# Performance work log

Measured on AMD Instinct MI355X. Metric: run time of the kernel, lower is better.

Reference implementation:

```python
import jax, jax.numpy as jnp
import numpy as np

B, C, H, W = 4, 256, 64, 64
CH = C // 2  # inner channels


def setup_inputs() -> dict:
    key = jax.random.key(0)
    ks = jax.random.split(key, 9)
    s_in = 1.0 / np.sqrt(C)
    s_w = 1.0 / np.sqrt(CH)
    return {
        "x": jax.random.normal(ks[0], (B, C, H, W), dtype=jnp.float32),
        "theta_w": jax.random.normal(ks[1], (CH, C), dtype=jnp.float32) * s_in,
        "theta_b": jax.random.normal(ks[2], (CH,), dtype=jnp.float32) * s_in,
        "phi_w": jax.random.normal(ks[3], (CH, C), dtype=jnp.float32) * s_in,
        "phi_b": jax.random.normal(ks[4], (CH,), dtype=jnp.float32) * s_in,
        "g_w": jax.random.normal(ks[5], (CH, C), dtype=jnp.float32) * s_in,
        "g_b": jax.random.normal(ks[6], (CH,), dtype=jnp.float32) * s_in,
        "W_w": jax.random.normal(ks[7], (C, CH), dtype=jnp.float32) * s_w,
        "W_b": jax.random.normal(ks[8], (C,), dtype=jnp.float32) * s_w,
    }


def _proj(x_flat, w, b):
    # 1x1 conv == channel matmul; x_flat: [B, C, N] -> [B, O, N]
    return jnp.einsum("oc,bcn->bon", w, x_flat) + b[None, :, None]


def reference(x, theta_w, theta_b, phi_w, phi_b, g_w, g_b, W_w, W_b):
    b, c, h, w = x.shape
    n = h * w
    xf = x.reshape(b, c, n)
    theta = _proj(xf, theta_w, theta_b)  # [B, CH, N]
    phi = _proj(xf, phi_w, phi_b)        # [B, CH, N]
    g = _proj(xf, g_w, g_b)              # [B, CH, N]
    # scores[b,i,j] = theta[:, :, i] . phi[:, :, j]; softmax over j
    attn = jax.nn.softmax(jnp.einsum("bci,bcj->bij", theta, phi), axis=-1)
    # torch: bmm(g_x, attn) -> out[b,c,i] = sum_j g[b,c,j] * attn[b,j,i]
    out = jnp.einsum("bcj,bji->bci", g, attn)  # [B, CH, N]
    out = jnp.einsum("oc,bcn->bon", W_w, out) + W_b[None, :, None]
    return out.reshape(b, c, h, w) + x
```

## Files before the change

### kernel.cpp

```cpp
#include <hip/hip_runtime.h>
#include <hip/hip_bf16.h>
#include <math.h>

#define BB    4
#define CC    256
#define CHN   128
#define NN    4096

typedef short short8 __attribute__((ext_vector_type(8)));
typedef float f32x4  __attribute__((ext_vector_type(4)));
typedef float f32x16 __attribute__((ext_vector_type(16)));
typedef unsigned short u16;
typedef u16  us4 __attribute__((ext_vector_type(4)));

#define MFMA16(a, b, c) __builtin_amdgcn_mfma_f32_16x16x32_bf16((a), (b), (c), 0, 0, 0)
#define MFMA32(a, b, c) __builtin_amdgcn_mfma_f32_32x32x16_bf16((a), (b), (c), 0, 0, 0)
#define LOG2E 1.4426950408889634f

#if __has_builtin(__builtin_amdgcn_exp2f)
#define EXP2F(x) __builtin_amdgcn_exp2f(x)
#else
#define EXP2F(x) exp2f(x)
#endif
#if __has_builtin(__builtin_amdgcn_logf)
#define LOG2F(x) __builtin_amdgcn_logf(x)
#else
#define LOG2F(x) log2f(x)
#endif

static __device__ __forceinline__ u16 f2bf(float f) {
    union { float f; unsigned u; } v; v.f = f;
    unsigned r = v.u + 0x7FFFu + ((v.u >> 16) & 1u);
    return (u16)(r >> 16);
}
static __device__ __forceinline__ unsigned pkbf(float a, float b) {
    __hip_bfloat162 h = __float22bfloat162_rn(make_float2(a, b));
    return *reinterpret_cast<unsigned*>(&h);
}
static __device__ __forceinline__ int sw128(int row, int u) {
    return row * 128 + ((u ^ (row & 7)) << 3);
}

__global__ __launch_bounds__(256) void k_cvtw(
    const float* __restrict__ tw, const float* __restrict__ pw,
    const float* __restrict__ gw, const float* __restrict__ Ww,
    u16* __restrict__ wall)
{
    int idx = (blockIdx.x * 256 + threadIdx.x) * 4;
    const float* s = (idx < 32768) ? tw
                   : (idx < 65536) ? pw
                   : (idx < 98304) ? gw : Ww;
    float sc = (idx < 32768) ? LOG2E : 1.0f;
    float4 v = *(const float4*)(s + (idx & 32767));
    us4 r = { f2bf(v.x * sc), f2bf(v.y * sc), f2bf(v.z * sc), f2bf(v.w * sc) };
    *(us4*)(wall + idx) = r;
}

__global__ __launch_bounds__(512) void k_proj(
    const float* __restrict__ x, const u16* __restrict__ wall,
    const float* __restrict__ tb, const float* __restrict__ pb,
    const float* __restrict__ gbias,
    u16* __restrict__ tht, u16* __restrict__ pht, u16* __restrict__ gg)
{
    __shared__ u16 xs[64 * 264];
    __shared__ u16 gbuf[128 * 68];
    const int tid = threadIdx.x;
    const int n0  = blockIdx.x * 64;
    const int b   = blockIdx.y;
    const int ln  = tid & 15, q = (tid >> 4) & 3, wid = tid >> 6;
    const int ow  = wid & 1, nw = wid >> 1;

    for (int p = 0; p < 8; ++p) {
        int id = p * 512 + tid;
        int c = id >> 4, n4 = (id & 15) * 4;
        float4 xv = *(const float4*)(x + ((size_t)b * CC + c) * NN + n0 + n4);
        xs[(n4 + 0) * 264 + c] = f2bf(xv.x);
        xs[(n4 + 1) * 264 + c] = f2bf(xv.y);
        xs[(n4 + 2) * 264 + c] = f2bf(xv.z);
        xs[(n4 + 3) * 264 + c] = f2bf(xv.w);
    }
    __syncthreads();

    short8 bfr[8];
    #pragma unroll
    for (int ks = 0; ks < 8; ++ks)
        bfr[ks] = *(const short8*)(&xs[(nw * 16 + ln) * 264 + ks * 32 + q * 8]);

    for (int pr = 0; pr < 3; ++pr) {
        const u16* wsrc = wall + pr * 32768;
        f32x4 acc[4];
        #pragma unroll
        for (int oo = 0; oo < 4; ++oo) acc[oo] = (f32x4){0.f, 0.f, 0.f, 0.f};
        for (int ks = 0; ks < 8; ++ks) {
            short8 a[4];
            #pragma unroll
            for (int oo = 0; oo < 4; ++oo)
                a[oo] = *(const short8*)(wsrc + (size_t)(ow*64 + oo*16 + ln) * 256 + ks*32 + q*8);
            #pragma unroll
            for (int oo = 0; oo < 4; ++oo)
                acc[oo] = MFMA16(a[oo], bfr[ks], acc[oo]);
        }
        const float* bias = (pr == 0) ? tb : (pr == 1 ? pb : gbias);
        const float bsc = (pr == 0) ? LOG2E : 1.0f;
        if (pr < 2) {
            u16* dst = (pr == 0) ? tht : pht;
            const int n = n0 + nw * 16 + ln;
            #pragma unroll
            for (int oo = 0; oo < 4; ++oo) {
                int o = ow * 64 + oo * 16 + q * 4;
                float4 bv = *(const float4*)(bias + o);
                f32x4 v = acc[oo];
                uint2 r = { pkbf(v.x + bv.x * bsc, v.y + bv.y * bsc),
                            pkbf(v.z + bv.z * bsc, v.w + bv.w * bsc) };
                *(uint2*)(dst + ((size_t)b * NN + n) * CHN + o) = r;
            }
        } else {
            const int nl = nw * 16 + ln;
            #pragma unroll
            for (int oo = 0; oo < 4; ++oo) {
                int o = ow * 64 + oo * 16 + q * 4;
                float4 bv = *(const float4*)(bias + o);
                f32x4 v = acc[oo];
                gbuf[(o + 0) * 68 + nl] = f2bf(v.x + bv.x);
                gbuf[(o + 1) * 68 + nl] = f2bf(v.y + bv.y);
                gbuf[(o + 2) * 68 + nl] = f2bf(v.z + bv.z);
                gbuf[(o + 3) * 68 + nl] = f2bf(v.w + bv.w);
            }
            __syncthreads();
            for (int p = 0; p < 4; ++p) {
                int id = p * 512 + tid;
                int c = id >> 4, n4 = (id & 15) * 4;
                us4 r = *(const us4*)(&gbuf[c * 68 + n4]);
                *(us4*)(gg + ((size_t)b * CHN + c) * NN + n0 + n4) = r;
            }
        }
    }
}

__global__ __launch_bounds__(512, 2) void k_rowsum(
    const u16* __restrict__ tht, const u16* __restrict__ pht,
    float* __restrict__ Z)
{
    __shared__ u16 ph_s[2][128 * 128];
    const int tid = threadIdx.x;
    const int j0  = blockIdx.x * 256;
    const int i00 = blockIdx.y * 1024;
    const int b   = blockIdx.z;
    const int l   = tid & 63, w = tid >> 6;
    const int lm  = l & 31, lh = l >> 5;
    const u16* thb = tht + (size_t)b * NN * CHN;
    const u16* phb = pht + (size_t)b * NN * CHN;

    short8 ar[8];
    #pragma unroll
    for (int ks = 0; ks < 8; ++ks)
        ar[ks] = *(const short8*)(thb + (size_t)(j0 + w*32 + lm) * CHN + ks*16 + lh*8);

    for (int p = 0; p < 4; ++p) {
        int id = p * 512 + tid;
        int row = id >> 4, u = id & 15;
        short8 v = *(const short8*)(phb + (size_t)(i00 + row) * CHN + u * 8);
        *(short8*)(&ph_s[0][sw128(row, u)]) = v;
    }

    float zp[16];
    #pragma unroll
    for (int r = 0; r < 16; ++r) zp[r] = 0.f;

    for (int is = 0; is < 8; ++is) {
        __syncthreads();
        if (is < 7) {
            for (int p = 0; p < 4; ++p) {
                int id = p * 512 + tid;
                int row = id >> 4, u = id & 15;
                short8 v = *(const short8*)(phb + (size_t)(i00 + (is+1)*128 + row) * CHN + u * 8);
                *(short8*)(&ph_s[(is + 1) & 1][sw128(row, u)]) = v;
            }
        }
        const u16* cur = ph_s[is & 1];

        #pragma unroll
        for (int ii = 0; ii < 4; ++ii) {
            f32x16 s;
            #pragma unroll
            for (int r = 0; r < 16; ++r) s[r] = 0.f;
            #pragma unroll
            for (int ks = 0; ks < 8; ++ks) {
                short8 bfrag = *(const short8*)(&cur[sw128(ii*32 + lm, ks*2 + lh)]);
                s = MFMA32(ar[ks], bfrag, s);
            }
            #pragma unroll
            for (int r = 0; r < 16; ++r) zp[r] += EXP2F(s[r]);
        }
    }

    float zr[16];
    #pragma unroll
    for (int r = 0; r < 16; ++r) {
        float v = zp[r];
        v += __shfl_xor(v, 1);
        v += __shfl_xor(v, 2);
        v += __shfl_xor(v, 4);
        v += __shfl_xor(v, 8);
        v += __shfl_xor(v, 16);
        zr[r] = v;
    }
    if (lm == 0) {
        #pragma unroll
        for (int r = 0; r < 16; ++r) {
            int j = j0 + w*32 + (r & 3) + 8*(r >> 2) + 4*lh;
            atomicAdd(&Z[(size_t)b * NN + j], zr[r]);
        }
    }
}

__global__ __launch_bounds__(256) void k_log(
    const float* __restrict__ Z, float* __restrict__ L)
{
    int idx = (blockIdx.x * 256 + threadIdx.x) * 4;
    float4 z = *(const float4*)(Z + idx);
    float4 r = { -LOG2F(z.x), -LOG2F(z.y), -LOG2F(z.z), -LOG2F(z.w) };
    *(float4*)(L + idx) = r;
}

__global__ __launch_bounds__(512, 2) void k_attn(
    const u16* __restrict__ tht, const u16* __restrict__ pht,
    const u16* __restrict__ gg, const float* __restrict__ Lbuf,
    u16* __restrict__ innerT)
{
    __shared__ u16 th_s[2][128 * 128];
    __shared__ u16 g_s [2][128 * 128];
    const int tid = threadIdx.x;
    const int i0  = blockIdx.x * 256;
    const int jq  = blockIdx.y;
    const int b   = blockIdx.z;
    const int w   = tid >> 6;
    const int lm  = tid & 31, lh = (tid >> 5) & 1;

    const u16*  thb = tht + (size_t)b * NN * CHN;
    const u16*  ggb = gg  + (size_t)b * CHN * NN;
    const float* Lb = Lbuf + (size_t)b * NN;

    int srow[4], su[4];
    #pragma unroll
    for (int p = 0; p < 4; ++p) {
        int id = p * 512 + tid;
        srow[p] = id >> 4; su[p] = id & 15;
    }

    short8 phr[8];
    #pragma unroll
    for (int ks = 0; ks < 8; ++ks)
        phr[ks] = *(const short8*)(pht + ((size_t)b * NN + i0 + w*32 + lm) * CHN + ks*16 + lh*8);

    #pragma unroll
    for (int p = 0; p < 4; ++p) {
        short8 tv = *(const short8*)(thb + (size_t)(jq*1024 + srow[p]) * CHN + su[p] * 8);
        short8 gv = *(const short8*)(ggb + (size_t)srow[p] * NN + jq*1024 + su[p] * 8);
        *(short8*)(&th_s[0][sw128(srow[p], su[p])]) = tv;
        *(short8*)(&g_s [0][sw128(srow[p], su[p])]) = gv;
    }
    __syncthreads();

    f32x16 pacc[4];
    #pragma unroll
    for (int ct = 0; ct < 4; ++ct)
        #pragma unroll
        for (int r = 0; r < 16; ++r) pacc[ct][r] = 0.f;

    for (int s = 0; s < 8; ++s) {
        const int j0s = jq * 1024 + s * 128;
        const u16* thc = th_s[s & 1];
        const u16* gc  = g_s [s & 1];

        short8 thn[4], gn[4];
        if (s < 7) {
            #pragma unroll
            for (int p = 0; p < 4; ++p) {
                thn[p] = *(const short8*)(thb + (size_t)(j0s + 128 + srow[p]) * CHN + su[p] * 8);
                gn[p]  = *(const short8*)(ggb + (size_t)srow[p] * NN + j0s + 128 + su[p] * 8);
            }
        }

        #pragma unroll
        for (int jj = 0; jj < 4; ++jj) {
            f32x16 sv;
            #pragma unroll
            for (int rq = 0; rq < 4; ++rq) {
                float4 Lv = *(const float4*)(Lb + j0s + jj*32 + rq*8 + lh*4);
                sv[rq*4 + 0] = Lv.x; sv[rq*4 + 1] = Lv.y;
                sv[rq*4 + 2] = Lv.z; sv[rq*4 + 3] = Lv.w;
            }
            #pragma unroll
            for (int ks = 0; ks < 8; ++ks) {
                short8 a = *(const short8*)(&thc[sw128(jj*32 + lm, ks*2 + lh)]);
                sv = MFMA32(a, phr[ks], sv);
            }
            unsigned e0 = pkbf(EXP2F(sv[0]),  EXP2F(sv[1]));
            unsigned e1 = pkbf(EXP2F(sv[2]),  EXP2F(sv[3]));
            unsigned e2 = pkbf(EXP2F(sv[4]),  EXP2F(sv[5]));
            unsigned e3 = pkbf(EXP2F(sv[6]),  EXP2F(sv[7]));
            unsigned e4 = pkbf(EXP2F(sv[8]),  EXP2F(sv[9]));
            unsigned e5 = pkbf(EXP2F(sv[10]), EXP2F(sv[11]));
            unsigned e6 = pkbf(EXP2F(sv[12]), EXP2F(sv[13]));
            unsigned e7 = pkbf(EXP2F(sv[14]), EXP2F(sv[15]));
            unsigned s0 = __shfl_xor(e0, 32), s1 = __shfl_xor(e1, 32);
            unsigned s2 = __shfl_xor(e2, 32), s3 = __shfl_xor(e3, 32);
            unsigned s4 = __shfl_xor(e4, 32), s5 = __shfl_xor(e5, 32);
            unsigned s6 = __shfl_xor(e6, 32), s7 = __shfl_xor(e7, 32);
            union { unsigned u[4]; short8 v; } f[2];
            f[0].u[0] = lh ? s2 : e0;  f[0].u[1] = lh ? s3 : e1;
            f[0].u[2] = lh ? e2 : s0;  f[0].u[3] = lh ? e3 : s1;
            f[1].u[0] = lh ? s6 : e4;  f[1].u[1] = lh ? s7 : e5;
            f[1].u[2] = lh ? e6 : s4;  f[1].u[3] = lh ? e7 : s5;
            #pragma unroll
            for (int h = 0; h < 2; ++h) {
                #pragma unroll
                for (int ct = 0; ct < 4; ++ct) {
                    short8 ag = *(const short8*)(&gc[sw128(ct*32 + lm, jj*4 + h*2 + lh)]);
                    pacc[ct] = MFMA32(ag, f[h].v, pacc[ct]);
                }
            }
        }

        if (s < 7) {
            const int nb = (s + 1) & 1;
            #pragma unroll
            for (int p = 0; p < 4; ++p) {
                *(short8*)(&th_s[nb][sw128(srow[p], su[p])]) = thn[p];
                *(short8*)(&g_s [nb][sw128(srow[p], su[p])]) = gn[p];
            }
        }
        __syncthreads();
    }

    u16* dst = innerT + ((size_t)jq * BB + b) * (size_t)NN * CHN;
    const int i = i0 + w*32 + lm;
    #pragma unroll
    for (int ct = 0; ct < 4; ++ct) {
        #pragma unroll
        for (int rq = 0; rq < 4; ++rq) {
            const int c0 = ct*32 + rq*8 + lh*4;
            uint2 r = { pkbf(pacc[ct][rq*4+0], pacc[ct][rq*4+1]),
                        pkbf(pacc[ct][rq*4+2], pacc[ct][rq*4+3]) };
            *(uint2*)(dst + (size_t)i * CHN + c0) = r;
        }
    }
}

__global__ __launch_bounds__(512, 2) void k_final(
    const u16* __restrict__ innerT, const float* __restrict__ x,
    const u16* __restrict__ Wwbf, const float* __restrict__ Wb,
    float* __restrict__ out)
{
    __shared__ u16 w_s[256 * 128];
    __shared__ u16 a_s[64 * 128];
    const int tid = threadIdx.x;
    const int n0  = blockIdx.x * 64;
    const int b   = blockIdx.y;
    const int l   = tid & 63, w = tid >> 6;
    const int lm  = l & 31, lh = l >> 5;

    for (int p = 0; p < 8; ++p) {
        int id = p * 512 + tid;
        int row = id >> 4, u = id & 15;
        *(short8*)(&w_s[sw128(row, u)]) = *(const short8*)(Wwbf + (size_t)row * CHN + u * 8);
    }
    __syncthreads();

    short8 aw[8];
    #pragma unroll
    for (int ks = 0; ks < 8; ++ks)
        aw[ks] = *(const short8*)(&w_s[sw128(w*32 + lm, ks*2 + lh)]);

    f32x16 acc[2];
    #pragma unroll
    for (int nt = 0; nt < 2; ++nt)
        #pragma unroll
        for (int r = 0; r < 16; ++r) acc[nt][r] = 0.f;

    for (int jq = 0; jq < 4; ++jq) {
        __syncthreads();
        for (int p = 0; p < 2; ++p) {
            int id = p * 512 + tid;
            int row = id >> 4, u = id & 15;
            *(short8*)(&a_s[sw128(row, u)]) =
                *(const short8*)(innerT + (((size_t)jq * BB + b) * NN + n0 + row) * CHN + u * 8);
        }
        __syncthreads();
        #pragma unroll
        for (int ks = 0; ks < 8; ++ks) {
            short8 bn[2];
            #pragma unroll
            for (int nt = 0; nt < 2; ++nt)
                bn[nt] = *(const short8*)(&a_s[sw128(nt*32 + lm, ks*2 + lh)]);
            acc[0] = MFMA32(aw[ks], bn[0], acc[0]);
            acc[1] = MFMA32(aw[ks], bn[1], acc[1]);
        }
    }

    #pragma unroll
    for (int nt = 0; nt < 2; ++nt) {
        const int n = n0 + nt*32 + lm;
        #pragma unroll
        for (int r = 0; r < 16; ++r) {
            const int o = w*32 + (r & 3) + 8*(r >> 2) + 4*lh;
            const size_t idx = ((size_t)b * CC + o) * NN + n;
            out[idx] = acc[nt][r] + Wb[o] + x[idx];
        }
    }
}

extern "C" void kernel_launch(void* const* d_in, const int* in_sizes, int n_in,
                              void* d_out, int out_size, void* d_ws, size_t ws_size,
                              hipStream_t stream)
{
    const float* x  = (const float*)d_in[0];
    const float* tw = (const float*)d_in[1];
    const float* tb = (const float*)d_in[2];
    const float* pw = (const float*)d_in[3];
    const float* pb = (const float*)d_in[4];
    const float* gw = (const float*)d_in[5];
    const float* gb = (const float*)d_in[6];
    const float* Ww = (const float*)d_in[7];
    const float* Wb = (const float*)d_in[8];
    float* out = (float*)d_out;

    char* p = (char*)d_ws;
    const size_t proj_u16 = (size_t)BB * NN * CHN;
    u16*   tht    = (u16*)p;   p += proj_u16 * 2;
    u16*   pht    = (u16*)p;   p += proj_u16 * 2;
    u16*   gg     = (u16*)p;   p += proj_u16 * 2;
    u16*   wall   = (u16*)p;   p += (size_t)131072 * 2;
    float* Z      = (float*)p; p += (size_t)BB * NN * 4;
    float* Lbuf   = (float*)p; p += (size_t)BB * NN * 4;
    u16*   innerT = (u16*)p;

    hipMemsetAsync(Z, 0, (size_t)BB * NN * sizeof(float), stream);
    k_cvtw  <<<128, 256, 0, stream>>>(tw, pw, gw, Ww, wall);
    k_proj  <<<dim3(64, BB), 512, 0, stream>>>(x, wall, tb, pb, gb, tht, pht, gg);
    k_rowsum<<<dim3(16, 4, BB), 512, 0, stream>>>(tht, pht, Z);
    k_log   <<<16, 256, 0, stream>>>(Z, Lbuf);
    k_attn  <<<dim3(16, 4, BB), 512, 0, stream>>>(tht, pht, gg, Lbuf, innerT);
    k_final <<<dim3(64, BB), 512, 0, stream>>>(innerT, x, wall + 98304, Wb, out);
}
```

Measured before the change: 191.3 us.

## Retile attention kernel with 2x i-reuse, j-split waves, and direct global-to-LDS loads

Each wave now owns 64 query rows split into two 32-row halves, and waves are split into two groups over the j sub-tiles, so every theta/g LDS fragment feeds two MFMAs. The two j-groups' partial accumulators are reduced through shared memory before the bf16 store. Tile loads switch from register staging to global_load_lds direct copies, which frees registers and drops the LDS store pass. The cost is doubled accumulator registers (pacc 4x2) and an extra LDS reduction plus barrier at the end.

```diff
diff --git a/kernel.cpp b/kernel.cpp
--- a/kernel.cpp
+++ b/kernel.cpp
@@ -40,6 +40,32 @@
 static __device__ __forceinline__ int sw128(int row, int u) {
     return row * 128 + ((u ^ (row & 7)) << 3);
 }
+static __device__ __forceinline__ void gload16(const u16* g, u16* l) {
+    __builtin_amdgcn_global_load_lds(
+        (const __attribute__((address_space(1))) void*)g,
+        (__attribute__((address_space(3))) void*)l, 16, 0, 0);
+}
+
+typedef union { unsigned u[4]; short8 v; } bfrag;
+
+#define REPACK(sv, f) do { \
+    unsigned e0 = pkbf(EXP2F(sv[0]),  EXP2F(sv[1])); \
+    unsigned e1 = pkbf(EXP2F(sv[2]),  EXP2F(sv[3])); \
+    unsigned e2 = pkbf(EXP2F(sv[4]),  EXP2F(sv[5])); \
+    unsigned e3 = pkbf(EXP2F(sv[6]),  EXP2F(sv[7])); \
+    unsigned e4 = pkbf(EXP2F(sv[8]),  EXP2F(sv[9])); \
+    unsigned e5 = pkbf(EXP2F(sv[10]), EXP2F(sv[11])); \
+    unsigned e6 = pkbf(EXP2F(sv[12]), EXP2F(sv[13])); \
+    unsigned e7 = pkbf(EXP2F(sv[14]), EXP2F(sv[15])); \
+    unsigned q0 = __shfl_xor(e0, 32), q1 = __shfl_xor(e1, 32); \
+    unsigned q2 = __shfl_xor(e2, 32), q3 = __shfl_xor(e3, 32); \
+    unsigned q4 = __shfl_xor(e4, 32), q5 = __shfl_xor(e5, 32); \
+    unsigned q6 = __shfl_xor(e6, 32), q7 = __shfl_xor(e7, 32); \
+    f[0].u[0] = lh ? q2 : e0;  f[0].u[1] = lh ? q3 : e1; \
+    f[0].u[2] = lh ? e2 : q0;  f[0].u[3] = lh ? e3 : q1; \
+    f[1].u[0] = lh ? q6 : e4;  f[1].u[1] = lh ? q7 : e5; \
+    f[1].u[2] = lh ? e6 : q4;  f[1].u[3] = lh ? e7 : q5; \
+} while (0)
 
 __global__ __launch_bounds__(256) void k_cvtw(
     const float* __restrict__ tw, const float* __restrict__ pw,
@@ -228,123 +254,133 @@
     const u16* __restrict__ gg, const float* __restrict__ Lbuf,
     u16* __restrict__ innerT)
 {
-    __shared__ u16 th_s[2][128 * 128];
-    __shared__ u16 g_s [2][128 * 128];
+    __shared__ u16 smem[4][128 * 128];
     const int tid = threadIdx.x;
     const int i0  = blockIdx.x * 256;
     const int jq  = blockIdx.y;
     const int b   = blockIdx.z;
     const int w   = tid >> 6;
+    const int iw  = w & 3;
+    const int jw  = w >> 2;
     const int lm  = tid & 31, lh = (tid >> 5) & 1;
 
     const u16*  thb = tht + (size_t)b * NN * CHN;
     const u16*  ggb = gg  + (size_t)b * CHN * NN;
     const float* Lb = Lbuf + (size_t)b * NN;
 
-    int srow[4], su[4];
+    int offT[4], offG[4];
     #pragma unroll
     for (int p = 0; p < 4; ++p) {
-        int id = p * 512 + tid;
-        srow[p] = id >> 4; su[p] = id & 15;
-    }
-
-    short8 phr[8];
-    #pragma unroll
-    for (int ks = 0; ks < 8; ++ks)
-        phr[ks] = *(const short8*)(pht + ((size_t)b * NN + i0 + w*32 + lm) * CHN + ks*16 + lh*8);
+        int row = p * 32 + (tid >> 4);
+        int u   = (tid & 15) ^ (row & 7);
+        offT[p] = row * CHN + u * 8;
+        offG[p] = row * NN  + u * 8;
+    }
+
+    short8 phr[2][8];
+    #pragma unroll
+    for (int ih = 0; ih < 2; ++ih)
+        #pragma unroll
+        for (int ks = 0; ks < 8; ++ks)
+            phr[ih][ks] = *(const short8*)(pht +
+                ((size_t)b * NN + i0 + iw*64 + ih*32 + lm) * CHN + ks*16 + lh*8);
 
     #pragma unroll
     for (int p = 0; p < 4; ++p) {
-        short8 tv = *(const short8*)(thb + (size_t)(jq*1024 + srow[p]) * CHN + su[p] * 8);
-        short8 gv = *(const short8*)(ggb + (size_t)srow[p] * NN + jq*1024 + su[p] * 8);
-        *(short8*)(&th_s[0][sw128(srow[p], su[p])]) = tv;
-        *(short8*)(&g_s [0][sw128(srow[p], su[p])]) = gv;
+        gload16(thb + (size_t)(jq * 1024) * CHN + offT[p], &smem[0][p*4096 + (w << 9)]);
+        gload16(ggb + jq * 1024 + offG[p],                 &smem[2][p*4096 + (w << 9)]);
     }
     __syncthreads();
 
-    f32x16 pacc[4];
+    f32x16 pacc[4][2];
     #pragma unroll
     for (int ct = 0; ct < 4; ++ct)
         #pragma unroll
-        for (int r = 0; r < 16; ++r) pacc[ct][r] = 0.f;
+        for (int ih = 0; ih < 2; ++ih)
+            #pragma unroll
+            for (int r = 0; r < 16; ++r) pacc[ct][ih][r] = 0.f;
 
     for (int s = 0; s < 8; ++s) {
         const int j0s = jq * 1024 + s * 128;
-        const u16* thc = th_s[s & 1];
-        const u16* gc  = g_s [s & 1];
-
-        short8 thn[4], gn[4];
+        const u16* thc = smem[s & 1];
+        const u16* gc  = smem[2 + (s & 1)];
+
         if (s < 7) {
+            const int nb = (s + 1) & 1;
             #pragma unroll
             for (int p = 0; p < 4; ++p) {
-                thn[p] = *(const short8*)(thb + (size_t)(j0s + 128 + srow[p]) * CHN + su[p] * 8);
-                gn[p]  = *(const short8*)(ggb + (size_t)srow[p] * NN + j0s + 128 + su[p] * 8);
-            }
-        }
-
-        #pragma unroll
-        for (int jj = 0; jj < 4; ++jj) {
-            f32x16 sv;
+                gload16(thb + (size_t)(j0s + 128) * CHN + offT[p], &smem[nb][p*4096 + (w << 9)]);
+                gload16(ggb + (j0s + 128) + offG[p],               &smem[2 + nb][p*4096 + (w << 9)]);
+            }
+        }
+
+        #pragma unroll
+        for (int jx = 0; jx < 2; ++jx) {
+            const int jj = jw * 2 + jx;
+            f32x16 sv0;
             #pragma unroll
             for (int rq = 0; rq < 4; ++rq) {
                 float4 Lv = *(const float4*)(Lb + j0s + jj*32 + rq*8 + lh*4);
-                sv[rq*4 + 0] = Lv.x; sv[rq*4 + 1] = Lv.y;
-                sv[rq*4 + 2] = Lv.z; sv[rq*4 + 3] = Lv.w;
-            }
+                sv0[rq*4 + 0] = Lv.x; sv0[rq*4 + 1] = Lv.y;
+                sv0[rq*4 + 2] = Lv.z; sv0[rq*4 + 3] = Lv.w;
+            }
+            f32x16 sv1 = sv0;
             #pragma unroll
             for (int ks = 0; ks < 8; ++ks) {
                 short8 a = *(const short8*)(&thc[sw128(jj*32 + lm, ks*2 + lh)]);
-                sv = MFMA32(a, phr[ks], sv);
-            }
-            unsigned e0 = pkbf(EXP2F(sv[0]),  EXP2F(sv[1]));
-            unsigned e1 = pkbf(EXP2F(sv[2]),  EXP2F(sv[3]));
-            unsigned e2 = pkbf(EXP2F(sv[4]),  EXP2F(sv[5]));
-            unsigned e3 = pkbf(EXP2F(sv[6]),  EXP2F(sv[7]));
-            unsigned e4 = pkbf(EXP2F(sv[8]),  EXP2F(sv[9]));
-            unsigned e5 = pkbf(EXP2F(sv[10]), EXP2F(sv[11]));
-            unsigned e6 = pkbf(EXP2F(sv[12]), EXP2F(sv[13]));
-            unsigned e7 = pkbf(EXP2F(sv[14]), EXP2F(sv[15]));
-            unsigned s0 = __shfl_xor(e0, 32), s1 = __shfl_xor(e1, 32);
-            unsigned s2 = __shfl_xor(e2, 32), s3 = __shfl_xor(e3, 32);
-            unsigned s4 = __shfl_xor(e4, 32), s5 = __shfl_xor(e5, 32);
-            unsigned s6 = __shfl_xor(e6, 32), s7 = __shfl_xor(e7, 32);
-            union { unsigned u[4]; short8 v; } f[2];
-            f[0].u[0] = lh ? s2 : e0;  f[0].u[1] = lh ? s3 : e1;
-            f[0].u[2] = lh ? e2 : s0;  f[0].u[3] = lh ? e3 : s1;
-            f[1].u[0] = lh ? s6 : e4;  f[1].u[1] = lh ? s7 : e5;
-            f[1].u[2] = lh ? e6 : s4;  f[1].u[3] = lh ? e7 : s5;
+                sv0 = MFMA32(a, phr[0][ks], sv0);
+                sv1 = MFMA32(a, phr[1][ks], sv1);
+            }
+            bfrag fA[2], fB[2];
+            REPACK(sv0, fA);
+            REPACK(sv1, fB);
             #pragma unroll
             for (int h = 0; h < 2; ++h) {
                 #pragma unroll
                 for (int ct = 0; ct < 4; ++ct) {
                     short8 ag = *(const short8*)(&gc[sw128(ct*32 + lm, jj*4 + h*2 + lh)]);
-                    pacc[ct] = MFMA32(ag, f[h].v, pacc[ct]);
+                    pacc[ct][0] = MFMA32(ag, fA[h].v, pacc[ct][0]);
+                    pacc[ct][1] = MFMA32(ag, fB[h].v, pacc[ct][1]);
                 }
             }
         }
-
-        if (s < 7) {
-            const int nb = (s + 1) & 1;
-            #pragma unroll
-            for (int p = 0; p < 4; ++p) {
-                *(short8*)(&th_s[nb][sw128(srow[p], su[p])]) = thn[p];
-                *(short8*)(&g_s [nb][sw128(srow[p], su[p])]) = gn[p];
-            }
-        }
         __syncthreads();
     }
 
-    u16* dst = innerT + ((size_t)jq * BB + b) * (size_t)NN * CHN;
-    const int i = i0 + w*32 + lm;
-    #pragma unroll
-    for (int ct = 0; ct < 4; ++ct) {
-        #pragma unroll
-        for (int rq = 0; rq < 4; ++rq) {
-            const int c0 = ct*32 + rq*8 + lh*4;
-            uint2 r = { pkbf(pacc[ct][rq*4+0], pacc[ct][rq*4+1]),
-                        pkbf(pacc[ct][rq*4+2], pacc[ct][rq*4+3]) };
-            *(uint2*)(dst + (size_t)i * CHN + c0) = r;
-        }
+    float* fb = (float*)smem;
+    if (jw == 1) {
+        #pragma unroll
+        for (int ct = 0; ct < 4; ++ct)
+            #pragma unroll
+            for (int ih = 0; ih < 2; ++ih) {
+                const int il = ih*32 + lm;
+                #pragma unroll
+                for (int rq = 0; rq < 4; ++rq) {
+                    const int c4 = ct*8 + rq*2 + lh;
+                    f32x4 v = { pacc[ct][ih][rq*4+0], pacc[ct][ih][rq*4+1],
+                                pacc[ct][ih][rq*4+2], pacc[ct][ih][rq*4+3] };
+                    *(f32x4*)(fb + iw*8192 + il*128 + ((c4 ^ (il & 7)) << 2)) = v;
+                }
+            }
+    }
+    __syncthreads();
+    if (jw == 0) {
+        u16* dst = innerT + ((size_t)jq * BB + b) * (size_t)NN * CHN;
+        #pragma unroll
+        for (int ct = 0; ct < 4; ++ct)
+            #pragma unroll
+            for (int ih = 0; ih < 2; ++ih) {
+                const int il = ih*32 + lm;
+                const int i  = i0 + iw*64 + il;
+                #pragma unroll
+                for (int rq = 0; rq < 4; ++rq) {
+                    const int c4 = ct*8 + rq*2 + lh;
+                    f32x4 v = *(const f32x4*)(fb + iw*8192 + il*128 + ((c4 ^ (il & 7)) << 2));
+                    uint2 r = { pkbf(pacc[ct][ih][rq*4+0] + v[0], pacc[ct][ih][rq*4+1] + v[1]),
+                                pkbf(pacc[ct][ih][rq*4+2] + v[2], pacc[ct][ih][rq*4+3] + v[3]) };
+                    *(uint2*)(dst + (size_t)i * CHN + ct*32 + rq*8 + lh*4) = r;
+                }
+            }
     }
 }
 
```

Result: slower. 216.8 us (+13.3%).

## Use direct global-to-LDS loads and permlane32 swap in attention kernel

Applied to the files above, without the earlier changes.

Replaces the register-staged prefetch of theta and g tiles with global_load_lds 16-byte direct copies into shared memory. The XOR swizzle is applied to the global source address so the LDS layout stays the same. This removes the register buffers and the separate LDS store pass, which should ease VGPR pressure and issue overhead. The exp/repack step also switches from shuffles plus selects to permlane32_swap when the builtin is available.

```diff
diff --git a/kernel.cpp b/kernel.cpp
--- a/kernel.cpp
+++ b/kernel.cpp
@@ -40,6 +40,53 @@
 static __device__ __forceinline__ int sw128(int row, int u) {
     return row * 128 + ((u ^ (row & 7)) << 3);
 }
+static __device__ __forceinline__ void gload16(const u16* g, u16* l) {
+    __builtin_amdgcn_global_load_lds(
+        (const __attribute__((address_space(1))) void*)g,
+        (__attribute__((address_space(3))) void*)l, 16, 0, 0);
+}
+
+typedef union { unsigned u[4]; short8 v; } bfrag;
+
+#if __has_builtin(__builtin_amdgcn_permlane32_swap)
+#define REPACK(sv, f) do { \
+    unsigned e0 = pkbf(EXP2F(sv[0]),  EXP2F(sv[1])); \
+    unsigned e1 = pkbf(EXP2F(sv[2]),  EXP2F(sv[3])); \
+    unsigned e2 = pkbf(EXP2F(sv[4]),  EXP2F(sv[5])); \
+    unsigned e3 = pkbf(EXP2F(sv[6]),  EXP2F(sv[7])); \
+    unsigned e4 = pkbf(EXP2F(sv[8]),  EXP2F(sv[9])); \
+    unsigned e5 = pkbf(EXP2F(sv[10]), EXP2F(sv[11])); \
+    unsigned e6 = pkbf(EXP2F(sv[12]), EXP2F(sv[13])); \
+    unsigned e7 = pkbf(EXP2F(sv[14]), EXP2F(sv[15])); \
+    auto r02 = __builtin_amdgcn_permlane32_swap(e0, e2, false, false); \
+    auto r13 = __builtin_amdgcn_permlane32_swap(e1, e3, false, false); \
+    auto r46 = __builtin_amdgcn_permlane32_swap(e4, e6, false, false); \
+    auto r57 = __builtin_amdgcn_permlane32_swap(e5, e7, false, false); \
+    f[0].u[0] = r02[0]; f[0].u[1] = r13[0]; \
+    f[0].u[2] = r02[1]; f[0].u[3] = r13[1]; \
+    f[1].u[0] = r46[0]; f[1].u[1] = r57[0]; \
+    f[1].u[2] = r46[1]; f[1].u[3] = r57[1]; \
+} while (0)
+#else
+#define REPACK(sv, f) do { \
+    unsigned e0 = pkbf(EXP2F(sv[0]),  EXP2F(sv[1])); \
+    unsigned e1 = pkbf(EXP2F(sv[2]),  EXP2F(sv[3])); \
+    unsigned e2 = pkbf(EXP2F(sv[4]),  EXP2F(sv[5])); \
+    unsigned e3 = pkbf(EXP2F(sv[6]),  EXP2F(sv[7])); \
+    unsigned e4 = pkbf(EXP2F(sv[8]),  EXP2F(sv[9])); \
+    unsigned e5 = pkbf(EXP2F(sv[10]), EXP2F(sv[11])); \
+    unsigned e6 = pkbf(EXP2F(sv[12]), EXP2F(sv[13])); \
+    unsigned e7 = pkbf(EXP2F(sv[14]), EXP2F(sv[15])); \
+    unsigned q0 = __shfl_xor(e0, 32), q1 = __shfl_xor(e1, 32); \
+    unsigned q2 = __shfl_xor(e2, 32), q3 = __shfl_xor(e3, 32); \
+    unsigned q4 = __shfl_xor(e4, 32), q5 = __shfl_xor(e5, 32); \
+    unsigned q6 = __shfl_xor(e6, 32), q7 = __shfl_xor(e7, 32); \
+    f[0].u[0] = lh ? q2 : e0;  f[0].u[1] = lh ? q3 : e1; \
+    f[0].u[2] = lh ? e2 : q0;  f[0].u[3] = lh ? e3 : q1; \
+    f[1].u[0] = lh ? q6 : e4;  f[1].u[1] = lh ? q7 : e5; \
+    f[1].u[2] = lh ? e6 : q4;  f[1].u[3] = lh ? e7 : q5; \
+} while (0)
+#endif
 
 __global__ __launch_bounds__(256) void k_cvtw(
     const float* __restrict__ tw, const float* __restrict__ pw,
@@ -241,11 +288,13 @@
     const u16*  ggb = gg  + (size_t)b * CHN * NN;
     const float* Lb = Lbuf + (size_t)b * NN;
 
-    int srow[4], su[4];
+    int offT[4], offG[4];
     #pragma unroll
     for (int p = 0; p < 4; ++p) {
-        int id = p * 512 + tid;
-        srow[p] = id >> 4; su[p] = id & 15;
+        int row = p * 32 + (tid >> 4);
+        int u   = (tid & 15) ^ (row & 7);
+        offT[p] = row * CHN + u * 8;
+        offG[p] = row * NN  + u * 8;
     }
 
     short8 phr[8];
@@ -255,10 +304,8 @@
 
     #pragma unroll
     for (int p = 0; p < 4; ++p) {
-        short8 tv = *(const short8*)(thb + (size_t)(jq*1024 + srow[p]) * CHN + su[p] * 8);
-        short8 gv = *(const short8*)(ggb + (size_t)srow[p] * NN + jq*1024 + su[p] * 8);
-        *(short8*)(&th_s[0][sw128(srow[p], su[p])]) = tv;
-        *(short8*)(&g_s [0][sw128(srow[p], su[p])]) = gv;
+        gload16(thb + (size_t)(jq * 1024) * CHN + offT[p], &th_s[0][0] + p*4096 + (w << 9));
+        gload16(ggb + jq * 1024 + offG[p],                 &g_s [0][0] + p*4096 + (w << 9));
     }
     __syncthreads();
 
@@ -273,12 +320,12 @@
         const u16* thc = th_s[s & 1];
         const u16* gc  = g_s [s & 1];
 
-        short8 thn[4], gn[4];
         if (s < 7) {
+            const int nb = (s + 1) & 1;
             #pragma unroll
             for (int p = 0; p < 4; ++p) {
-                thn[p] = *(const short8*)(thb + (size_t)(j0s + 128 + srow[p]) * CHN + su[p] * 8);
-                gn[p]  = *(const short8*)(ggb + (size_t)srow[p] * NN + j0s + 128 + su[p] * 8);
+                gload16(thb + (size_t)(j0s + 128) * CHN + offT[p], &th_s[nb][0] + p*4096 + (w << 9));
+                gload16(ggb + (j0s + 128) + offG[p],               &g_s [nb][0] + p*4096 + (w << 9));
             }
         }
 
@@ -296,23 +343,8 @@
                 short8 a = *(const short8*)(&thc[sw128(jj*32 + lm, ks*2 + lh)]);
                 sv = MFMA32(a, phr[ks], sv);
             }
-            unsigned e0 = pkbf(EXP2F(sv[0]),  EXP2F(sv[1]));
-            unsigned e1 = pkbf(EXP2F(sv[2]),  EXP2F(sv[3]));
-            unsigned e2 = pkbf(EXP2F(sv[4]),  EXP2F(sv[5]));
-            unsigned e3 = pkbf(EXP2F(sv[6]),  EXP2F(sv[7]));
-            unsigned e4 = pkbf(EXP2F(sv[8]),  EXP2F(sv[9]));
-            unsigned e5 = pkbf(EXP2F(sv[10]), EXP2F(sv[11]));
-            unsigned e6 = pkbf(EXP2F(sv[12]), EXP2F(sv[13]));
-            unsigned e7 = pkbf(EXP2F(sv[14]), EXP2F(sv[15]));
-            unsigned s0 = __shfl_xor(e0, 32), s1 = __shfl_xor(e1, 32);
-            unsigned s2 = __shfl_xor(e2, 32), s3 = __shfl_xor(e3, 32);
-            unsigned s4 = __shfl_xor(e4, 32), s5 = __shfl_xor(e5, 32);
-            unsigned s6 = __shfl_xor(e6, 32), s7 = __shfl_xor(e7, 32);
-            union { unsigned u[4]; short8 v; } f[2];
-            f[0].u[0] = lh ? s2 : e0;  f[0].u[1] = lh ? s3 : e1;
-            f[0].u[2] = lh ? e2 : s0;  f[0].u[3] = lh ? e3 : s1;
-            f[1].u[0] = lh ? s6 : e4;  f[1].u[1] = lh ? s7 : e5;
-            f[1].u[2] = lh ? e6 : s4;  f[1].u[3] = lh ? e7 : s5;
+            bfrag f[2];
+            REPACK(sv, f);
             #pragma unroll
             for (int h = 0; h < 2; ++h) {
                 #pragma unroll
@@ -320,15 +352,6 @@
                     short8 ag = *(const short8*)(&gc[sw128(ct*32 + lm, jj*4 + h*2 + lh)]);
                     pacc[ct] = MFMA32(ag, f[h].v, pacc[ct]);
                 }
-            }
-        }
-
-        if (s < 7) {
-            const int nb = (s + 1) & 1;
-            #pragma unroll
-            for (int p = 0; p < 4; ++p) {
-                *(short8*)(&th_s[nb][sw128(srow[p], su[p])]) = thn[p];
-                *(short8*)(&g_s [nb][sw128(srow[p], su[p])]) = gn[p];
             }
         }
         __syncthreads();
```

After: 189.1 us. About the same (-1.2%).
